# Optimization experiments

Measured on AMD Instinct MI355X. Metric: run time of the kernel, lower is better.

Reference implementation:

```python
import jax, jax.numpy as jnp
import numpy as np

T, N, B, CIN, COUT = 12, 2048, 16, 64, 64
EMB = 16


def normalize_adj(A):
    # relu -> add self-loops -> symmetric degree normalization
    A = jax.nn.relu(A) + jnp.eye(A.shape[0], dtype=A.dtype)
    d_inv_sqrt = jnp.clip(A.sum(axis=-1), 1e-12, None) ** -0.5
    return d_inv_sqrt[:, None] * A * d_inv_sqrt[None, :]


def setup_inputs() -> dict:
    key = jax.random.key(0)
    ks = jax.random.split(key, 6)
    return {
        "x": jax.random.normal(ks[0], (T * N, B, CIN), dtype=jnp.float32),
        "A_static": jax.random.uniform(ks[1], (N, N), dtype=jnp.float32),
        "node_emb1": jax.random.normal(ks[2], (N, EMB), dtype=jnp.float32),
        "node_emb2": jax.random.normal(ks[3], (EMB, N), dtype=jnp.float32),
        "alpha": jnp.array([0.5], dtype=jnp.float32),
        "W_fc": jax.random.normal(ks[4], (CIN, 2 * COUT), dtype=jnp.float32) * (1.0 / np.sqrt(CIN)),
        "b_fc": jax.random.normal(ks[5], (2 * COUT,), dtype=jnp.float32) * 0.01,
    }


def reference(x, A_static, node_emb1, node_emb2, alpha, W_fc, b_fc):
    # Adaptive unified graph
    A_adaptive = jax.nn.softmax(jax.nn.relu(node_emb1 @ node_emb2), axis=-1)
    a = jax.nn.sigmoid(alpha[0])
    A = a * normalize_adj(A_static) + (1.0 - a) * normalize_adj(A_adaptive)
    # block_diag(A, T) @ x over leading dim == per-timestep batched matmul
    xt = x.reshape(T, N, B, CIN)
    y = jnp.einsum('nm,tmbc->tnbc', A, xt).reshape(T * N, B, CIN)
    # GLU gated linear layer
    lhs_rhs = y @ W_fc + b_fc
    lhs, rhs = lhs_rhs[..., :COUT], lhs_rhs[..., COUT:]
    return lhs * jax.nn.sigmoid(rhs)
```

## Files before the change

kernel.cpp:

```cpp
#include <hip/hip_runtime.h>
#include <hip/hip_bf16.h>
#include <stdint.h>

#define T_DIM 12
#define N_DIM 2048
#define B_DIM 16
#define C_IN  64
#define C_OUT 64
#define EMB   16
#define P_DIM 1024

typedef __attribute__((ext_vector_type(8))) short short8;
typedef __attribute__((ext_vector_type(4))) float f32x4;

static __device__ __forceinline__ unsigned short f2bf(float f) {
  union { float f; uint32_t u; } v; v.f = f;
  uint32_t u = v.u;
  return (unsigned short)((u + 0x7fffu + ((u >> 16) & 1u)) >> 16);
}

static __device__ __forceinline__ float sigf(float x) {
  return __builtin_amdgcn_rcpf(1.0f + __expf(-x));
}

static __device__ __forceinline__ void gload16(const void* g, void* l) {
  __builtin_amdgcn_global_load_lds(
      (const __attribute__((address_space(1))) unsigned int*)g,
      (__attribute__((address_space(3))) unsigned int*)l, 16, 0, 0);
}

template<bool MAX>
static __device__ __forceinline__ float block_red(float v, float* red) {
  #pragma unroll
  for (int o = 32; o > 0; o >>= 1) {
    float t = __shfl_down(v, o, 64);
    v = MAX ? fmaxf(v, t) : (v + t);
  }
  __syncthreads();
  if ((threadIdx.x & 63) == 0) red[threadIdx.x >> 6] = v;
  __syncthreads();
  float r = red[0];
  #pragma unroll
  for (int w = 1; w < 4; ++w) r = MAX ? fmaxf(r, red[w]) : (r + red[w]);
  return r;
}

__launch_bounds__(256)
__global__ void k_stats(const float* __restrict__ As, const float* __restrict__ E1,
                        const float* __restrict__ E2, float* __restrict__ dinv,
                        float* __restrict__ mx, float* __restrict__ se) {
  int n = blockIdx.x, tid = threadIdx.x;
  __shared__ float e1s[EMB];
  __shared__ float red[4];
  if (tid < EMB) e1s[tid] = E1[n * EMB + tid];
  __syncthreads();

  float rs = 0.f;
  #pragma unroll
  for (int i = 0; i < N_DIM / 256; ++i)
    rs += fmaxf(As[(size_t)n * N_DIM + i * 256 + tid], 0.f);

  float p[8];
  #pragma unroll
  for (int i = 0; i < 8; ++i) {
    int m = i * 256 + tid;
    float d = 0.f;
    #pragma unroll
    for (int e = 0; e < EMB; ++e) d += e1s[e] * E2[e * N_DIM + m];
    p[i] = fmaxf(d, 0.f);
  }
  float lmx = p[0];
  #pragma unroll
  for (int i = 1; i < 8; ++i) lmx = fmaxf(lmx, p[i]);
  float gmx = block_red<true>(lmx, red);
  float ls = 0.f;
  #pragma unroll
  for (int i = 0; i < 8; ++i) ls += expf(p[i] - gmx);
  float gse = block_red<false>(ls, red);
  float grs = block_red<false>(rs, red);
  if (tid == 0) {
    dinv[n] = rsqrtf(fmaxf(grs + 1.0f, 1e-12f));
    mx[n] = gmx;
    se[n] = gse;
  }
}

__launch_bounds__(256)
__global__ void k_wt(const float* __restrict__ W, unsigned short* __restrict__ WT) {
  int q = blockIdx.x * 256 + threadIdx.x;
  int j = q >> 6, c = q & 63;
  WT[q] = f2bf(W[c * 128 + j]);
}

__launch_bounds__(256)
__global__ void k_abuild(const float* __restrict__ As, const float* __restrict__ E1,
                         const float* __restrict__ E2, const float* __restrict__ alpha,
                         const float* __restrict__ dinv, const float* __restrict__ mx,
                         const float* __restrict__ se, unsigned short* __restrict__ A) {
  int n = blockIdx.x, tid = threadIdx.x;
  __shared__ float e1s[EMB];
  if (tid < EMB) e1s[tid] = E1[n * EMB + tid];
  __syncthreads();
  float a = sigf(alpha[0]);
  float di_n = dinv[n], m_n = mx[n], inv_se = 1.f / se[n];
  float ca = a, cb = (1.f - a) * 0.5f;
  #pragma unroll
  for (int i = 0; i < 8; ++i) {
    int m = i * 256 + tid;
    float d = 0.f;
    #pragma unroll
    for (int e = 0; e < EMB; ++e) d += e1s[e] * E2[e * N_DIM + m];
    float soft = expf(fmaxf(d, 0.f) - m_n) * inv_se;
    float idm = (m == n) ? 1.f : 0.f;
    float sv = fmaxf(As[(size_t)n * N_DIM + m], 0.f) + idm;
    float val = ca * di_n * dinv[m] * sv + cb * (soft + idm);
    A[(size_t)n * N_DIM + m] = f2bf(val);
  }
}

__launch_bounds__(256)
__global__ void k_xt(const float* __restrict__ x, unsigned short* __restrict__ XT) {
  __shared__ float tile[64 * 65];
  int bid = blockIdx.x;
  int t = bid >> 9;
  int rem = bid & 511;
  int mt = rem >> 4, pt = rem & 15;
  int m0 = mt * 64, p0 = pt * 64;
  int tid = threadIdx.x;
  #pragma unroll
  for (int i = 0; i < 4; ++i) {
    int lin = i * 256 + tid;
    int mm = lin >> 4;
    int pp4 = lin & 15;
    const float4 v = *(const float4*)&x[(size_t)(t * N_DIM + m0 + mm) * P_DIM + p0 + pp4 * 4];
    tile[(pp4 * 4 + 0) * 65 + mm] = v.x;
    tile[(pp4 * 4 + 1) * 65 + mm] = v.y;
    tile[(pp4 * 4 + 2) * 65 + mm] = v.z;
    tile[(pp4 * 4 + 3) * 65 + mm] = v.w;
  }
  __syncthreads();
  #pragma unroll
  for (int i = 0; i < 2; ++i) {
    int lin = i * 256 + tid;
    int pp = lin >> 3;
    int mmb = (lin & 7) * 8;
    union { unsigned short s[8]; uint4 u; } pk;
    #pragma unroll
    for (int q = 0; q < 8; ++q) pk.s[q] = f2bf(tile[pp * 65 + mmb + q]);
    *(uint4*)&XT[(size_t)t * P_DIM * N_DIM + (size_t)(p0 + pp) * N_DIM + m0 + mmb] = pk.u;
  }
}

__launch_bounds__(256, 3)
__global__ void k_gemm(const unsigned short* __restrict__ A,
                       const unsigned short* __restrict__ XT,
                       const unsigned short* __restrict__ WT,
                       const float* __restrict__ bfc,
                       float* __restrict__ out) {
  __shared__ __align__(16) char lds[32768];

  int v = blockIdx.x;
  int mb = v & 15;
  int pf = v >> 4;
  int n0 = mb * 128;
  int p0f = pf * 128;
  int t = p0f >> 10;
  int b0 = (p0f & 1023) >> 6;

  int tid = threadIdx.x;
  int lane = tid & 63, wid = tid >> 6;
  int wr = wid >> 1, wc = wid & 1;
  int wsd = wid * 1024;

  int srow = tid >> 3;
  int scol = ((tid & 7) ^ (srow & 7)) * 8;
  const unsigned short* gA = A + (size_t)(n0 + srow) * N_DIM + scol;
  const unsigned short* gB = XT + (size_t)(p0f + srow) * N_DIM + scol;

  int rsw = ((lane >> 4) * 16) ^ ((lane & 7) << 4);
  int faoff = (wr * 64 + (lane & 15)) * 128 + rsw;
  int fboff = (wc * 64 + (lane & 15)) * 128 + rsw;

  f32x4 acc[4][4];
  #pragma unroll
  for (int m = 0; m < 4; ++m)
    #pragma unroll
    for (int n = 0; n < 4; ++n) acc[m][n] = (f32x4){0.f, 0.f, 0.f, 0.f};

  for (int j = 0; j < 32; ++j) {
    size_t ko = (size_t)j * 64;
    #pragma unroll
    for (int s = 0; s < 4; ++s) gload16(gA + s * 65536 + ko, lds + s * 4096 + wsd);
    #pragma unroll
    for (int s = 0; s < 4; ++s) gload16(gB + s * 65536 + ko, lds + 16384 + s * 4096 + wsd);
    __syncthreads();

    short8 fa[4][2], fb[4][2];
    #pragma unroll
    for (int mi = 0; mi < 4; ++mi)
      #pragma unroll
      for (int kk = 0; kk < 2; ++kk)
        fa[mi][kk] = *(const short8*)(lds + ((faoff + mi * 2048) ^ (kk * 64)));
    #pragma unroll
    for (int ni = 0; ni < 4; ++ni)
      #pragma unroll
      for (int kk = 0; kk < 2; ++kk)
        fb[ni][kk] = *(const short8*)(lds + 16384 + ((fboff + ni * 2048) ^ (kk * 64)));
    #pragma unroll
    for (int mi = 0; mi < 4; ++mi)
      #pragma unroll
      for (int ni = 0; ni < 4; ++ni) {
        acc[mi][ni] = __builtin_amdgcn_mfma_f32_16x16x32_bf16(fa[mi][0], fb[ni][0], acc[mi][ni], 0, 0, 0);
        acc[mi][ni] = __builtin_amdgcn_mfma_f32_16x16x32_bf16(fa[mi][1], fb[ni][1], acc[mi][ni], 0, 0, 0);
      }
    __syncthreads();
  }

  #pragma unroll
  for (int m = 0; m < 4; ++m) {
    #pragma unroll
    for (int n = 0; n < 4; ++n) {
      #pragma unroll
      for (int reg = 0; reg < 4; ++reg) {
        int rl = wr * 64 + m * 16 + ((lane >> 4) << 2) + reg;
        int cin = n * 16 + (lane & 15);
        int nb = rl * 2 + wc;
        int byte = nb * 128 + ((cin * 2) ^ ((nb & 7) << 4));
        *(unsigned short*)(lds + byte) = f2bf(acc[m][n][reg]);
      }
    }
  }
  __syncthreads();

  short8 wf0[8], wf1[8];
  float bl[8];
  #pragma unroll
  for (int f2 = 0; f2 < 8; ++f2) {
    int jc = f2 * 16 + (lane & 15);
    wf0[f2] = *(const short8*)((const char*)WT + jc * 128 + (lane >> 4) * 16);
    wf1[f2] = *(const short8*)((const char*)WT + jc * 128 + 64 + (lane >> 4) * 16);
    bl[f2] = bfc[jc];
  }

  #pragma unroll
  for (int r2 = 0; r2 < 4; ++r2) {
    int row = wid * 64 + r2 * 16 + (lane & 15);
    int cb = ((lane >> 4) * 16) ^ ((row & 7) << 4);
    short8 a0 = *(const short8*)(lds + (row * 128 + cb));
    short8 a1 = *(const short8*)(lds + ((row * 128 + cb) ^ 64));
    f32x4 acc2[8];
    #pragma unroll
    for (int f2 = 0; f2 < 8; ++f2) {
      acc2[f2] = (f32x4){0.f, 0.f, 0.f, 0.f};
      acc2[f2] = __builtin_amdgcn_mfma_f32_16x16x32_bf16(a0, wf0[f2], acc2[f2], 0, 0, 0);
      acc2[f2] = __builtin_amdgcn_mfma_f32_16x16x32_bf16(a1, wf1[f2], acc2[f2], 0, 0, 0);
    }
    #pragma unroll
    for (int f2 = 0; f2 < 4; ++f2) {
      #pragma unroll
      for (int reg = 0; reg < 4; ++reg) {
        int nb = wid * 64 + r2 * 16 + ((lane >> 4) << 2) + reg;
        float zl = acc2[f2][reg] + bl[f2];
        float zr = acc2[f2 + 4][reg] + bl[f2 + 4];
        float ov = zl * sigf(zr);
        int n = n0 + (nb >> 1);
        int b = b0 + (nb & 1);
        int co = f2 * 16 + (lane & 15);
        out[(size_t)((t * N_DIM + n) * B_DIM + b) * C_OUT + co] = ov;
      }
    }
  }
}

extern "C" void kernel_launch(void* const* d_in, const int* in_sizes, int n_in,
                              void* d_out, int out_size, void* d_ws, size_t ws_size,
                              hipStream_t stream) {
  const float* x  = (const float*)d_in[0];
  const float* As = (const float*)d_in[1];
  const float* E1 = (const float*)d_in[2];
  const float* E2 = (const float*)d_in[3];
  const float* al = (const float*)d_in[4];
  const float* W  = (const float*)d_in[5];
  const float* bf = (const float*)d_in[6];
  float* out = (float*)d_out;

  char* ws = (char*)d_ws;
  unsigned short* XT = (unsigned short*)ws;
  unsigned short* Ab = (unsigned short*)(ws + 50331648);
  unsigned short* WT = (unsigned short*)(ws + 58720256);
  float* dinv = (float*)(ws + 58736640);
  float* mx   = (float*)(ws + 58744832);
  float* se   = (float*)(ws + 58753024);

  k_stats<<<dim3(2048), dim3(256), 0, stream>>>(As, E1, E2, dinv, mx, se);
  k_wt<<<dim3(32), dim3(256), 0, stream>>>(W, WT);
  k_abuild<<<dim3(2048), dim3(256), 0, stream>>>(As, E1, E2, al, dinv, mx, se, Ab);
  k_xt<<<dim3(6144), dim3(256), 0, stream>>>(x, XT);
  k_gemm<<<dim3(1536), dim3(256), 0, stream>>>(Ab, XT, WT, bf, out);
}
```

Baseline: 184.3 us.

## Merge prep kernels into one launch and compute softmax stats inside abuild

The x transpose/convert, the A_static row-degree pass and the W transpose now run as block ranges of a single prep kernel. The softmax max and sum are computed inside k_abuild, so the adaptive logits are no longer computed twice and the mx/se round trip through global memory is gone. This removes two kernel launches and one full recomputation of the embedding product, at the cost of a more heterogeneous prep kernel.

```diff
diff --git a/kernel.cpp b/kernel.cpp
--- a/kernel.cpp
+++ b/kernel.cpp
@@ -46,20 +46,65 @@
 }
 
 __launch_bounds__(256)
-__global__ void k_stats(const float* __restrict__ As, const float* __restrict__ E1,
-                        const float* __restrict__ E2, float* __restrict__ dinv,
-                        float* __restrict__ mx, float* __restrict__ se) {
+__global__ void k_prep(const float* __restrict__ x, unsigned short* __restrict__ XT,
+                       const float* __restrict__ As, float* __restrict__ dinv,
+                       const float* __restrict__ W, unsigned short* __restrict__ WT) {
+  __shared__ float smf[64 * 65];
+  int bid = blockIdx.x;
+  int tid = threadIdx.x;
+
+  if (bid < 6144) {
+    int t = bid >> 9;
+    int rem = bid & 511;
+    int mt = rem >> 4, pt = rem & 15;
+    int m0 = mt * 64, p0 = pt * 64;
+    #pragma unroll
+    for (int i = 0; i < 4; ++i) {
+      int lin = i * 256 + tid;
+      int mm = lin >> 4;
+      int pp4 = lin & 15;
+      const float4 v = *(const float4*)&x[(size_t)(t * N_DIM + m0 + mm) * P_DIM + p0 + pp4 * 4];
+      smf[(pp4 * 4 + 0) * 65 + mm] = v.x;
+      smf[(pp4 * 4 + 1) * 65 + mm] = v.y;
+      smf[(pp4 * 4 + 2) * 65 + mm] = v.z;
+      smf[(pp4 * 4 + 3) * 65 + mm] = v.w;
+    }
+    __syncthreads();
+    #pragma unroll
+    for (int i = 0; i < 2; ++i) {
+      int lin = i * 256 + tid;
+      int pp = lin >> 3;
+      int mmb = (lin & 7) * 8;
+      union { unsigned short s[8]; uint4 u; } pk;
+      #pragma unroll
+      for (int q = 0; q < 8; ++q) pk.s[q] = f2bf(smf[pp * 65 + mmb + q]);
+      *(uint4*)&XT[(size_t)t * P_DIM * N_DIM + (size_t)(p0 + pp) * N_DIM + m0 + mmb] = pk.u;
+    }
+  } else if (bid < 8192) {
+    int n = bid - 6144;
+    float rs = 0.f;
+    #pragma unroll
+    for (int i = 0; i < N_DIM / 256; ++i)
+      rs += fmaxf(As[(size_t)n * N_DIM + i * 256 + tid], 0.f);
+    float grs = block_red<false>(rs, smf);
+    if (tid == 0) dinv[n] = rsqrtf(fmaxf(grs + 1.0f, 1e-12f));
+  } else {
+    int q = (bid - 8192) * 256 + tid;
+    int j = q >> 6, c = q & 63;
+    WT[q] = f2bf(W[c * 128 + j]);
+  }
+}
+
+__launch_bounds__(256)
+__global__ void k_abuild(const float* __restrict__ As, const float* __restrict__ E1,
+                         const float* __restrict__ E2, const float* __restrict__ alpha,
+                         const float* __restrict__ dinv, unsigned short* __restrict__ A) {
   int n = blockIdx.x, tid = threadIdx.x;
   __shared__ float e1s[EMB];
   __shared__ float red[4];
   if (tid < EMB) e1s[tid] = E1[n * EMB + tid];
   __syncthreads();
 
-  float rs = 0.f;
-  #pragma unroll
-  for (int i = 0; i < N_DIM / 256; ++i)
-    rs += fmaxf(As[(size_t)n * N_DIM + i * 256 + tid], 0.f);
-
   float p[8];
   #pragma unroll
   for (int i = 0; i < 8; ++i) {
@@ -77,77 +122,18 @@
   #pragma unroll
   for (int i = 0; i < 8; ++i) ls += expf(p[i] - gmx);
   float gse = block_red<false>(ls, red);
-  float grs = block_red<false>(rs, red);
-  if (tid == 0) {
-    dinv[n] = rsqrtf(fmaxf(grs + 1.0f, 1e-12f));
-    mx[n] = gmx;
-    se[n] = gse;
-  }
-}
-
-__launch_bounds__(256)
-__global__ void k_wt(const float* __restrict__ W, unsigned short* __restrict__ WT) {
-  int q = blockIdx.x * 256 + threadIdx.x;
-  int j = q >> 6, c = q & 63;
-  WT[q] = f2bf(W[c * 128 + j]);
-}
-
-__launch_bounds__(256)
-__global__ void k_abuild(const float* __restrict__ As, const float* __restrict__ E1,
-                         const float* __restrict__ E2, const float* __restrict__ alpha,
-                         const float* __restrict__ dinv, const float* __restrict__ mx,
-                         const float* __restrict__ se, unsigned short* __restrict__ A) {
-  int n = blockIdx.x, tid = threadIdx.x;
-  __shared__ float e1s[EMB];
-  if (tid < EMB) e1s[tid] = E1[n * EMB + tid];
-  __syncthreads();
+
   float a = sigf(alpha[0]);
-  float di_n = dinv[n], m_n = mx[n], inv_se = 1.f / se[n];
+  float di_n = dinv[n], inv_se = 1.f / gse;
   float ca = a, cb = (1.f - a) * 0.5f;
   #pragma unroll
   for (int i = 0; i < 8; ++i) {
     int m = i * 256 + tid;
-    float d = 0.f;
-    #pragma unroll
-    for (int e = 0; e < EMB; ++e) d += e1s[e] * E2[e * N_DIM + m];
-    float soft = expf(fmaxf(d, 0.f) - m_n) * inv_se;
+    float soft = expf(p[i] - gmx) * inv_se;
     float idm = (m == n) ? 1.f : 0.f;
     float sv = fmaxf(As[(size_t)n * N_DIM + m], 0.f) + idm;
     float val = ca * di_n * dinv[m] * sv + cb * (soft + idm);
     A[(size_t)n * N_DIM + m] = f2bf(val);
-  }
-}
-
-__launch_bounds__(256)
-__global__ void k_xt(const float* __restrict__ x, unsigned short* __restrict__ XT) {
-  __shared__ float tile[64 * 65];
-  int bid = blockIdx.x;
-  int t = bid >> 9;
-  int rem = bid & 511;
-  int mt = rem >> 4, pt = rem & 15;
-  int m0 = mt * 64, p0 = pt * 64;
-  int tid = threadIdx.x;
-  #pragma unroll
-  for (int i = 0; i < 4; ++i) {
-    int lin = i * 256 + tid;
-    int mm = lin >> 4;
-    int pp4 = lin & 15;
-    const float4 v = *(const float4*)&x[(size_t)(t * N_DIM + m0 + mm) * P_DIM + p0 + pp4 * 4];
-    tile[(pp4 * 4 + 0) * 65 + mm] = v.x;
-    tile[(pp4 * 4 + 1) * 65 + mm] = v.y;
-    tile[(pp4 * 4 + 2) * 65 + mm] = v.z;
-    tile[(pp4 * 4 + 3) * 65 + mm] = v.w;
-  }
-  __syncthreads();
-  #pragma unroll
-  for (int i = 0; i < 2; ++i) {
-    int lin = i * 256 + tid;
-    int pp = lin >> 3;
-    int mmb = (lin & 7) * 8;
-    union { unsigned short s[8]; uint4 u; } pk;
-    #pragma unroll
-    for (int q = 0; q < 8; ++q) pk.s[q] = f2bf(tile[pp * 65 + mmb + q]);
-    *(uint4*)&XT[(size_t)t * P_DIM * N_DIM + (size_t)(p0 + pp) * N_DIM + m0 + mmb] = pk.u;
   }
 }
 
@@ -289,12 +275,8 @@
   unsigned short* Ab = (unsigned short*)(ws + 50331648);
   unsigned short* WT = (unsigned short*)(ws + 58720256);
   float* dinv = (float*)(ws + 58736640);
-  float* mx   = (float*)(ws + 58744832);
-  float* se   = (float*)(ws + 58753024);
-
-  k_stats<<<dim3(2048), dim3(256), 0, stream>>>(As, E1, E2, dinv, mx, se);
-  k_wt<<<dim3(32), dim3(256), 0, stream>>>(W, WT);
-  k_abuild<<<dim3(2048), dim3(256), 0, stream>>>(As, E1, E2, al, dinv, mx, se, Ab);
-  k_xt<<<dim3(6144), dim3(256), 0, stream>>>(x, XT);
+
+  k_prep<<<dim3(8224), dim3(256), 0, stream>>>(x, XT, As, dinv, W, WT);
+  k_abuild<<<dim3(2048), dim3(256), 0, stream>>>(As, E1, E2, al, dinv, Ab);
   k_gemm<<<dim3(1536), dim3(256), 0, stream>>>(Ab, XT, WT, bf, out);
 }
```

Measured after the change: 165.4 us. 1.11x faster.
